# Kernel tuning notes

Measured on AMD Instinct MI355X. Metric: run time of the kernel, lower is better.

Reference implementation:

```python
import jax, jax.numpy as jnp
import numpy as np

MC = 16384
N_STEPS = 120
PERIOD = 30
N_MAT = 4
N_STR = 21
WIDTH_DIFF = 50
WIDTH_VAN = 30
WIDTH_EXO = 20
N_HIDDEN = 3  # n_layers=4 -> input layer + 3 hidden layers + output layer
R = 0.05
TIMEGRID = jnp.asarray(np.linspace(0.0, 1.0, N_STEPS + 1).astype(np.float32))
STRIKES = jnp.asarray(np.linspace(0.8, 1.2, N_STR).astype(np.float32))


def _init_net(key, d_in, width, d_out):
    ks = jax.random.split(key, 6)
    f = lambda k, shape, fan: jax.random.normal(k, shape, jnp.float32) / np.sqrt(fan).astype(np.float32)
    return dict(
        W0=f(ks[0], (N_MAT, d_in, width), d_in),
        b0=f(ks[1], (N_MAT, width), width),
        hW=f(ks[2], (N_MAT, N_HIDDEN, width, width), width),
        hb=f(ks[3], (N_MAT, N_HIDDEN, width), width),
        Wo=f(ks[4], (N_MAT, width, d_out), width),
        bo=f(ks[5], (N_MAT, d_out), width),
    )


def setup_inputs() -> dict:
    key = jax.random.key(0)
    kz, kd, kv, ke = jax.random.split(key, 4)
    inp = {
        "S0": jnp.ones((1,), jnp.float32),
        "z": jax.random.normal(kz, (MC, N_STEPS), jnp.float32),
    }
    for name, net in (("d", _init_net(kd, 2, WIDTH_DIFF, 1)),
                      ("v", _init_net(kv, 2, WIDTH_VAN, N_STR * N_MAT)),
                      ("e", _init_net(ke, N_STEPS + 2, WIDTH_EXO, 1))):
        for pn, arr in net.items():
            inp[name + pn] = arr
    inp["MC_samples"] = MC
    inp["ind_T"] = N_STEPS
    inp["period_length"] = PERIOD
    return inp


def _mlp(x, W0, b0, hW, hb, Wo, bo, softplus_out):
    h = jax.nn.relu(x @ W0 + b0)
    for k in range(hW.shape[0]):  # static small number of hidden layers
        h = jax.nn.relu(h @ hW[k] + hb[k])
    y = h @ Wo + bo
    return jax.nn.softplus(y) if softplus_out else y


def _forward(S0, z, dW0, db0, dhW, dhb, dWo, dbo,
             vW0, vb0, vhW, vhb, vWo, vbo,
             eW0, eb0, ehW, ehb, eWo, ebo,
             MC_samples, ind_T, period_length, remat=False):
    sg = jax.lax.stop_gradient
    S_init = jnp.ones((MC_samples, 1), jnp.float32) * S0
    path0 = jnp.zeros((MC_samples, N_STEPS + 1), jnp.float32).at[:, 0].set(S_init[:, 0])
    zeros_mat = jnp.zeros((N_MAT, N_STR), jnp.float32)

    def step(carry, i):
        S_old, cv_v, cv_e, run_max, path, pv, pvv = carry
        idx = (i - 1) // period_length
        t0 = TIMEGRID[i - 1]
        h = TIMEGRID[i] - TIMEGRID[i - 1]
        sqh = jnp.sqrt(h)
        dWn = sqh * jax.lax.dynamic_slice_in_dim(z, i - 1, 1, 1)  # (MC,1)
        t = jnp.full_like(S_old, t0)
        diff = _mlp(jnp.concatenate([t, S_old], 1),
                    dW0[idx], db0[idx], dhW[idx], dhb[idx], dWo[idx], dbo[idx], True)
        Sd, diffd = sg(S_old), sg(diff)
        S_new = (S_old
                 + R * S_old * h / (1.0 + R * Sd * sqh)
                 + S_old * diff * dWn / (1.0 + Sd * diffd * sqh))
        disc = jnp.exp(-R * t0)
        cv_v = cv_v + disc * Sd * diffd * dWn * _mlp(
            jnp.concatenate([t, Sd], 1),
            vW0[idx], vb0[idx], vhW[idx], vhb[idx], vWo[idx], vbo[idx], False)
        cv_e = cv_e + disc * Sd * diffd * dWn * _mlp(
            jnp.concatenate([t, path], 1),
            eW0[idx], eb0[idx], ehW[idx], ehb[idx], eWo[idx], ebo[idx], False)
        path = jax.lax.dynamic_update_slice(path, sg(S_new), (0, i))
        run_max = jnp.maximum(run_max, S_new)
        # vanilla prices at maturities (i multiple of period_length)
        ind_m = i // period_length - 1
        disc_i = jnp.exp(-R * TIMEGRID[i])
        cv_row = jax.lax.dynamic_slice_in_dim(
            cv_v.reshape(MC_samples, N_MAT, N_STR), ind_m, 1, 1)[:, 0, :]
        pr = disc_i * jnp.maximum(S_new - STRIKES[None, :], 0.0) - cv_row  # (MC, N_STR)
        is_mat = (i % period_length) == 0
        pv = jnp.where(is_mat, jax.lax.dynamic_update_index_in_dim(pv, pr.mean(0), ind_m, 0), pv)
        pvv = jnp.where(is_mat, jax.lax.dynamic_update_index_in_dim(pvv, jnp.var(pr, axis=0, ddof=1), ind_m, 0), pvv)
        return (S_new, cv_v, cv_e, run_max, path, pv, pvv), None

    body = jax.checkpoint(step) if remat else step
    carry0 = (S_init,
              jnp.zeros((MC_samples, N_STR * N_MAT), jnp.float32),
              jnp.zeros((MC_samples, 1), jnp.float32),
              S_init, path0, zeros_mat, zeros_mat)
    (S_T, cv_v, cv_e, run_max, path, pv, pvv), _ = jax.lax.scan(
        body, carry0, jnp.arange(1, ind_T + 1))

    sgv = jax.lax.stop_gradient
    exotic = run_max - S_T
    discT = jnp.exp(-R * TIMEGRID[ind_T])
    e = discT * exotic
    error = sgv(e) - jnp.mean(sgv(e)) - sgv(cv_e)
    price_exo = e - cv_e
    return pv, pvv, price_exo, price_exo.mean(), jnp.var(price_exo, ddof=1), error


def reference(S0, z, dW0, db0, dhW, dhb, dWo, dbo,
              vW0, vb0, vhW, vhb, vWo, vbo,
              eW0, eb0, ehW, ehb, eWo, ebo,
              MC_samples, ind_T, period_length):
    return _forward(S0, z, dW0, db0, dhW, dhb, dWo, dbo,
                    vW0, vb0, vhW, vhb, vWo, vbo,
                    eW0, eb0, ehW, ehb, eWo, ebo,
                    MC_samples, ind_T, period_length)
```

## Files before the change

kernel.cpp:

```cpp
#include <hip/hip_runtime.h>
#include <hip/hip_bf16.h>
#include <math.h>

#define MC      16384
#define NSTEPS  120
#define PER     30
#define NMAT    4
#define NSTR    21
#define RRATE   0.05f
#define NBLK    1024
#define NSAMP   16
#define HSTEP   (1.0f/120.0f)
#define SQH     0.09128709291752769f

typedef short short8  __attribute__((ext_vector_type(8)));
typedef short short4v __attribute__((ext_vector_type(4)));
typedef float f32x4   __attribute__((ext_vector_type(4)));

#define WS_PRPART 0
#define WS_EPART  (NMAT*NSTR*2*NBLK)
#define WS_MEANE  (WS_EPART + NBLK)
#define WS_FRAGS  (WS_MEANE + 3)

#define OUT_PV    0
#define OUT_PVV   84
#define OUT_PEXO  168
#define OUT_MEAN  16552
#define OUT_VAR   16553
#define OUT_ERR   16554

__device__ __forceinline__ float tgridf(int i)  { return (float)i * HSTEP; }
__device__ __forceinline__ float strikef(int s) { return (float)(0.8 + (double)s * 0.02); }
__device__ __forceinline__ float softplusf(float x){
  return fmaxf(x, 0.0f) + __logf(1.0f + __expf(-fabsf(x)));
}
__device__ __forceinline__ unsigned short f2bf(float f){
  __hip_bfloat16 b = __float2bfloat16(f);
  return __builtin_bit_cast(unsigned short, b);
}
__device__ __forceinline__ float bf2f(unsigned short u){
  return __builtin_bit_cast(float, ((unsigned)u)<<16);
}
__device__ __forceinline__ int swaddr(int row, int slot, int inner){
  return row*256 + (((slot + row) & 15) << 4) + inner;
}
__device__ __forceinline__ short8 rdA(const unsigned short* H, int base, int lane){
  int addr = swaddr(lane&15, base + (lane>>4), 0);
  return *(const short8*)((const char*)H + addr);
}
__device__ __forceinline__ f32x4 mm(short8 a, short8 b, f32x4 c){
  return __builtin_amdgcn_mfma_f32_16x16x32_bf16(a, b, c, 0, 0, 0);
}
__device__ __forceinline__ void stD(unsigned short* H, int colbase, int lane,
                                    f32x4 acc, bool relu){
  int col  = colbase + (lane & 15);
  int slot = col >> 3, inner = (col & 7)*2;
  #pragma unroll
  for (int i2=0;i2<4;++i2){
    int rw = ((lane>>4)<<2) + i2;
    float v = acc[i2];
    if (relu) v = fmaxf(v, 0.0f);
    *(unsigned short*)((char*)H + swaddr(rw, slot, inner)) = f2bf(v);
  }
}
__device__ __forceinline__ short8 mkBd(const float* __restrict__ W, const float* __restrict__ bias,
                                       int n0, int kt, int lane){
  short8 r;
  int n = n0 + (lane&15);
  #pragma unroll
  for (int i2=0;i2<8;++i2){
    int k = kt*32 + ((lane>>4)<<3) + i2;
    float w;
    if (k<50)       w = (n<50)? W[k*50+n] : 0.f;
    else if (k==50) w = (n<50)? bias[n] : ((n==50)? 1.f : 0.f);
    else            w = 0.f;
    r[i2] = (short)f2bf(w);
  }
  return r;
}
__device__ __forceinline__ short8 mkBq(const float* __restrict__ W, const float* __restrict__ bias,
                                       int KV, int n0, int lane){
  short8 r;
  int n = n0 + (lane&15);
  #pragma unroll
  for (int i2=0;i2<8;++i2){
    int k = ((lane>>4)<<3) + i2;
    float w;
    if (k<KV)       w = (n<KV)? W[k*KV+n] : 0.f;
    else if (k==KV) w = (n<KV)? bias[n] : ((n==KV)? 1.f : 0.f);
    else            w = 0.f;
    r[i2] = (short)f2bf(w);
  }
  return r;
}

extern "C" __global__ void mk_frags(
    const float* __restrict__ dhW, const float* __restrict__ dhb,
    const float* __restrict__ vhW, const float* __restrict__ vhb,
    const float* __restrict__ ehW, const float* __restrict__ ehb,
    float* __restrict__ ws)
{
  const int bid = blockIdx.x;
  const int p   = bid / 36;
  const int fid = bid % 36;
  const int lane = threadIdx.x;
  short8 fr;
  if (fid < 24){
    int l = fid >> 3, nt = (fid >> 1) & 3, kt = fid & 1;
    fr = mkBd(dhW + p*7500 + l*2500, dhb + p*150 + l*50, nt*16, kt, lane);
  } else if (fid < 30){
    int q = fid - 24, l = q >> 1, nt = q & 1;
    fr = mkBq(vhW + p*2700 + l*900, vhb + p*90 + l*30, 30, nt*16, lane);
  } else {
    int q = fid - 30, l = q >> 1, nt = q & 1;
    fr = mkBq(ehW + p*1200 + l*400, ehb + p*60 + l*20, 20, nt*16, lane);
  }
  ((short8*)(ws + WS_FRAGS))[(p*36 + fid)*64 + lane] = fr;
}

extern "C" __global__ void __launch_bounds__(128,2) mc_main(
    const float* __restrict__ S0p, const float* __restrict__ z,
    const float* __restrict__ dW0, const float* __restrict__ db0,
    const float* __restrict__ dhW, const float* __restrict__ dhb,
    const float* __restrict__ dWo, const float* __restrict__ dbo,
    const float* __restrict__ vW0, const float* __restrict__ vb0,
    const float* __restrict__ vhW, const float* __restrict__ vhb,
    const float* __restrict__ vWo, const float* __restrict__ vbo,
    const float* __restrict__ eW0, const float* __restrict__ eb0,
    const float* __restrict__ ehW, const float* __restrict__ ehb,
    const float* __restrict__ eWo, const float* __restrict__ ebo,
    float* __restrict__ out, float* __restrict__ ws)
{
  __shared__ unsigned short Hb0[NSAMP*128];
  __shared__ unsigned short Hb1[NSAMP*128];
  __shared__ float vh3f[NSAMP*40];
  __shared__ float zper[NSAMP*30];
  __shared__ float eW0per[NMAT*600];
  __shared__ float dW0s[128];
  __shared__ float db0s[64];
  __shared__ float vW0s[64];
  __shared__ float vb0s[32];
  __shared__ float eW0ts[20];
  __shared__ float eb0s[20];
  __shared__ float dWoL[64];
  __shared__ float eWoL[32];
  __shared__ float dtab[PER];
  __shared__ float Sb[NSAMP], ebuf[NSAMP];
  __shared__ float part[84*2];

  const int tid  = threadIdx.x;
  const int lane = tid & 63;
  const int wid  = __builtin_amdgcn_readfirstlane(tid >> 6);
  const int blk  = blockIdx.x;
  const int r    = tid >> 3;
  const int cc   = tid & 7;

  const bool isv = (wid == 0);
  const int  ntA = wid*2, ntB = wid*2+1;

  const float S0v = S0p[0];
  float S = S0v, runmax = S0v, cvE = 0.f;
  f32x4 rr[3];
  #pragma unroll
  for (int q=0;q<3;++q){ rr[q][0]=0.f; rr[q][1]=0.f; rr[q][2]=0.f; rr[q][3]=0.f; }
  float aE[NMAT][4];
  #pragma unroll
  for (int mt2=0;mt2<NMAT;++mt2){ aE[mt2][0]=0.f; aE[mt2][1]=0.f; aE[mt2][2]=0.f; aE[mt2][3]=0.f; }
  float G_[4] = {0.f,0.f,0.f,0.f};

  #pragma unroll 1
  for (int p=0;p<NMAT;++p){
    for (int q=tid; q<NSAMP*30; q+=128){ int r2=q/30, c2=q%30; zper[q] = z[(size_t)(blk*NSAMP+r2)*NSTEPS + p*30 + c2]; }
    for (int q=tid; q<NMAT*600; q+=128){ int mat=q/600, k=q%600; eW0per[q] = eW0[mat*2440 + p*600 + 20 + k]; }
    { int rw = tid>>6, j = tid&63; dW0s[tid] = (j<50)? dW0[p*100 + rw*50 + j] : 0.f; }
    if (tid < 64) db0s[tid] = (tid<50)? db0[p*50+tid] : ((tid==50)? 1.f : 0.f);
    else { int idx = tid-64, rw = idx>>5, j = idx&31; vW0s[idx] = (j<30)? vW0[p*60 + rw*30 + j] : 0.f; }
    if (tid < 32)       vb0s[tid] = (tid<30)? vb0[p*30+tid] : ((tid==30)? 1.f : 0.f);
    else if (tid < 64){ int j=tid-32; if (j<20){ eW0ts[j]=eW0[p*2440+j]; eb0s[j]=eb0[p*20+j]; } }
    else { int j=tid-64; dWoL[j] = (j<50)? dWo[p*50+j] : 0.f; }
    if (tid < 32)       eWoL[tid] = (tid<20)? eWo[p*20+tid] : 0.f;
    else if (tid < 62){ int j=tid-32; dtab[j] = __expf(-RRATE * ((float)(p*PER+j) * HSTEP)); }

    const float dboS = dbo[p], eboS = ebo[p];
    const int fq0 = isv ? 24 : 30;

    __syncthreads();

    #pragma unroll 1
    for (int ii=1; ii<=PER; ++ii){
      const float t0  = tgridf(p*PER + ii - 1);

      const short8* FBp;
      { uintptr_t u = (uintptr_t)(ws + WS_FRAGS); asm volatile("" : "+s"(u));
        FBp = (const short8*)u + (size_t)p*36*64 + lane; }

      {
        short8 hv;
        #pragma unroll
        for (int k=0;k<8;++k){
          int j = cc*8 + k;
          float u = fmaxf(fmaf(t0, dW0s[j], fmaf(S, dW0s[64+j], db0s[j])), 0.f);
          hv[k] = (short)f2bf(u);
        }
        *(short8*)((char*)Hb0 + swaddr(r, cc, 0)) = hv;
        short4v vv;
        #pragma unroll
        for (int k=0;k<4;++k){
          int j = cc*4 + k;
          float u = fmaxf(fmaf(t0, vW0s[j], fmaf(S, vW0s[32+j], vb0s[j])), 0.f);
          vv[k] = (short)f2bf(u);
        }
        *(short4v*)((char*)Hb0 + swaddr(r, 8+(cc>>1), (cc&1)*8)) = vv;
        short4v ev = {0,0,0,0};
        if (cc < 5){
          const int o = (ii-1)*20 + cc*4;
          f32x4 w0 = *(const f32x4*)&eW0per[        o];
          f32x4 w1 = *(const f32x4*)&eW0per[ 600 +  o];
          f32x4 w2 = *(const f32x4*)&eW0per[1200 +  o];
          f32x4 w3 = *(const f32x4*)&eW0per[1800 +  o];
          #pragma unroll
          for (int k=0;k<4;++k){
            aE[0][k] = fmaf(S, w0[k], aE[0][k]);
            aE[1][k] = fmaf(S, w1[k], aE[1][k]);
            aE[2][k] = fmaf(S, w2[k], aE[2][k]);
            aE[3][k] = fmaf(S, w3[k], aE[3][k]);
            float a = (p==0)?aE[0][k]:(p==1)?aE[1][k]:(p==2)?aE[2][k]:aE[3][k];
            int j = cc*4 + k;
            float e0 = fmaxf(t0*eW0ts[j] + a + eb0s[j], 0.f);
            ev[k] = (short)f2bf(e0);
          }
        } else if (cc == 5){
          ev[0] = (short)0x3F80;
        }
        *(short4v*)((char*)Hb0 + swaddr(r, 12+(cc>>1), (cc&1)*8)) = ev;
      }
      __syncthreads();
      {
        short8 bA0 = FBp[(ntA*2+0)*64], bA1 = FBp[(ntA*2+1)*64];
        short8 bB0 = FBp[(ntB*2+0)*64], bB1 = FBp[(ntB*2+1)*64];
        short8 Bq0 = FBp[(fq0+0)*64],   Bq1 = FBp[(fq0+1)*64];
        short8 a0 = rdA(Hb0,0,lane), a1 = rdA(Hb0,4,lane);
        short8 aq = rdA(Hb0, isv?8:12, lane);
        f32x4 c0={0.f,0.f,0.f,0.f}, c1={0.f,0.f,0.f,0.f};
        c0=mm(a0,bA0,c0); c0=mm(a1,bA1,c0);
        c1=mm(a0,bB0,c1); c1=mm(a1,bB1,c1);
        stD(Hb1, ntA*16, lane, c0, true);
        stD(Hb1, ntB*16, lane, c1, true);
        f32x4 cq0={0.f,0.f,0.f,0.f}, cq1={0.f,0.f,0.f,0.f};
        cq0=mm(aq,Bq0,cq0); cq1=mm(aq,Bq1,cq1);
        stD(Hb1, (isv?64:96)+0,  lane, cq0, true);
        stD(Hb1, (isv?64:96)+16, lane, cq1, true);
      }
      __syncthreads();
      {
        short8 bA0 = FBp[(8+ntA*2+0)*64], bA1 = FBp[(8+ntA*2+1)*64];
        short8 bB0 = FBp[(8+ntB*2+0)*64], bB1 = FBp[(8+ntB*2+1)*64];
        short8 Bq0 = FBp[(fq0+2+0)*64],   Bq1 = FBp[(fq0+2+1)*64];
        short8 a0 = rdA(Hb1,0,lane), a1 = rdA(Hb1,4,lane);
        short8 aq = rdA(Hb1, isv?8:12, lane);
        f32x4 c0={0.f,0.f,0.f,0.f}, c1={0.f,0.f,0.f,0.f};
        c0=mm(a0,bA0,c0); c0=mm(a1,bA1,c0);
        c1=mm(a0,bB0,c1); c1=mm(a1,bB1,c1);
        stD(Hb0, ntA*16, lane, c0, true);
        stD(Hb0, ntB*16, lane, c1, true);
        f32x4 cq0={0.f,0.f,0.f,0.f}, cq1={0.f,0.f,0.f,0.f};
        cq0=mm(aq,Bq0,cq0); cq1=mm(aq,Bq1,cq1);
        stD(Hb0, (isv?64:96)+0,  lane, cq0, true);
        stD(Hb0, (isv?64:96)+16, lane, cq1, true);
      }
      __syncthreads();
      {
        short8 bA0 = FBp[(16+ntA*2+0)*64], bA1 = FBp[(16+ntA*2+1)*64];
        short8 bB0 = FBp[(16+ntB*2+0)*64], bB1 = FBp[(16+ntB*2+1)*64];
        short8 Bq0 = FBp[(fq0+4+0)*64],    Bq1 = FBp[(fq0+4+1)*64];
        short8 a0 = rdA(Hb0,0,lane), a1 = rdA(Hb0,4,lane);
        short8 aq = rdA(Hb0, isv?8:12, lane);
        f32x4 c0={0.f,0.f,0.f,0.f}, c1={0.f,0.f,0.f,0.f};
        c0=mm(a0,bA0,c0); c0=mm(a1,bA1,c0);
        c1=mm(a0,bB0,c1); c1=mm(a1,bB1,c1);
        stD(Hb1, ntA*16, lane, c0, true);
        stD(Hb1, ntB*16, lane, c1, true);
        f32x4 cq0={0.f,0.f,0.f,0.f}, cq1={0.f,0.f,0.f,0.f};
        cq0=mm(aq,Bq0,cq0); cq1=mm(aq,Bq1,cq1);
        if (isv){
          #pragma unroll
          for (int i2=0;i2<4;++i2){
            int r0 = ((lane>>4)<<2) + i2;
            vh3f[r0*40 +      (lane&15)] = fmaxf(cq0[i2], 0.f);
            vh3f[r0*40 + 16 + (lane&15)] = fmaxf(cq1[i2], 0.f);
          }
        } else {
          stD(Hb1, 96+0,  lane, cq0, true);
          stD(Hb1, 96+16, lane, cq1, true);
        }
      }
      __syncthreads();
      {
        float yp = 0.f;
        {
          short8 hv = *(const short8*)((const char*)Hb1 + swaddr(r, cc, 0));
          #pragma unroll
          for (int k=0;k<8;++k) yp = fmaf(bf2f((unsigned short)hv[k]), dWoL[cc*8+k], yp);
        }
        float yep = 0.f;
        if (cc < 5){
          short4v hv = *(const short4v*)((const char*)Hb1 + swaddr(r, 12+(cc>>1), (cc&1)*8));
          #pragma unroll
          for (int k=0;k<4;++k) yep = fmaf(bf2f((unsigned short)hv[k]), eWoL[cc*4+k], yep);
        }
        #pragma unroll
        for (int mk=1; mk<8; mk<<=1){ yp += __shfl_xor(yp, mk); yep += __shfl_xor(yep, mk); }
        const float y    = yp + dboS;
        const float diff = softplusf(y);
        const float zv   = zper[r*30 + (ii-1)];
        const float dWn  = SQH * zv;
        const float d1 = 1.f + (RRATE*SQH)*S;
        const float d2 = 1.f + S*diff*SQH;
        const float Snew = S + (RRATE*HSTEP)*S*__builtin_amdgcn_rcpf(d1)
                             + S*diff*dWn*__builtin_amdgcn_rcpf(d2);
        const float disc = dtab[ii-1];
        const float coef = disc * S * diff * dWn;
        cvE = fmaf(coef, yep + eboS, cvE);
        runmax = fmaxf(runmax, Snew);
        {
          f32x4 vv = *(const f32x4*)&vh3f[r*40 + cc*4];
          #pragma unroll
          for (int k=0;k<4;++k) G_[k] = fmaf(coef, vv[k], G_[k]);
        }
        S = Snew;

        if (ii==PER){
          short4v gv;
          #pragma unroll
          for (int k=0;k<4;++k){ gv[k] = (short)f2bf(G_[k]); G_[k] = 0.f; }
          *(short4v*)((char*)Hb0 + swaddr(r, cc>>1, (cc&1)*8)) = gv;
          if (cc==0) Sb[r] = S;
        }
      }

      if (ii==PER){
        __syncthreads();
        const float disc_i = __expf(-RRATE * ((float)(p+1) * 0.25f));
        const float* vWop = vWo + p*2520;
        const float* vbop = vbo + p*84;
        #pragma unroll
        for (int q3=0;q3<3;++q3){
          const int ntr = wid*3 + q3;
          short8 a = rdA(Hb0, 0, lane);
          const int col = ntr*16 + (lane&15);
          short8 bw;
          #pragma unroll
          for (int i2=0;i2<8;++i2){
            int k = ((lane>>4)<<3)+i2;
            float w = 0.f;
            if (col < 84){
              if (k < 30)       w = vWop[k*84+col];
              else if (k == 30) w = vbop[col];
            }
            bw[i2] = (short)f2bf(w);
          }
          f32x4 d4 = {0.f,0.f,0.f,0.f};
          d4 = mm(a,bw,d4);
          const int s = col - p*NSTR;
          const bool inr = (s>=0) && (s<NSTR) && (col<84);
          const float K = strikef(s);
          float ssum=0.f, ssq=0.f;
          #pragma unroll
          for (int i2=0;i2<4;++i2){
            int row = ((lane>>4)<<2) + i2;
            rr[q3][i2] += d4[i2];
            if (inr){
              float pr = disc_i*fmaxf(Sb[row]-K,0.f) - rr[q3][i2];
              ssum += pr; ssq = fmaf(pr,pr,ssq);
            }
          }
          ssum += __shfl_down(ssum,16); ssum += __shfl_down(ssum,32);
          ssq  += __shfl_down(ssq ,16); ssq  += __shfl_down(ssq ,32);
          if (inr && lane<16){
            part[col*2+0] = ssum;
            part[col*2+1] = ssq;
          }
        }
        __syncthreads();
        if (tid < NSTR){
          int cidx = p*NSTR + tid;
          ws[WS_PRPART + (cidx*2+0)*NBLK + blk] = part[cidx*2];
        } else if (tid >= 64 && tid < 64+NSTR){
          int cidx = p*NSTR + (tid-64);
          ws[WS_PRPART + (cidx*2+1)*NBLK + blk] = part[cidx*2+1];
        }
        __syncthreads();
      }
    }
  }

  if (cc==0){
    const float discT = __expf(-RRATE);
    const float e = discT * (runmax - S);
    out[OUT_PEXO + blk*NSAMP + r] = e - cvE;
    ebuf[r] = e;
  }
  __syncthreads();
  if (tid < 16){
    float se = ebuf[tid];
    se += __shfl_down(se,8); se += __shfl_down(se,4);
    se += __shfl_down(se,2); se += __shfl_down(se,1);
    if (tid==0) ws[WS_EPART + blk] = se;
  }
}

extern "C" __global__ void fin_pv(const float* __restrict__ ws, float* __restrict__ out){
  const int t = threadIdx.x;
  if (t >= NMAT*NSTR) return;
  float sum=0.0f, ssq=0.0f;
  for (int b=0;b<NBLK;++b){
    sum += ws[WS_PRPART + (t*2+0)*NBLK + b];
    ssq += ws[WS_PRPART + (t*2+1)*NBLK + b];
  }
  out[OUT_PV  + t] = sum * (1.0f/MC);
  out[OUT_PVV + t] = (ssq - sum*sum*(1.0f/MC)) * (1.0f/(MC-1));
}

extern "C" __global__ void fin_pe(float* out, float* ws){
  __shared__ float sA[4], sB[4], sC[4];
  const int t = threadIdx.x;
  float sum=0.0f, ssq=0.0f;
  for (int idx=t; idx<MC; idx+=256){
    const float v = out[OUT_PEXO+idx];
    sum += v; ssq = fmaf(v,v,ssq);
  }
  float es = 0.0f;
  for (int idx=t; idx<NBLK; idx+=256) es += ws[WS_EPART + idx];
  for (int o=32;o>0;o>>=1){
    sum += __shfl_down(sum,o);
    ssq += __shfl_down(ssq,o);
    es  += __shfl_down(es,o);
  }
  const int w=t>>6, lane=t&63;
  if (lane==0){ sA[w]=sum; sB[w]=ssq; sC[w]=es; }
  __syncthreads();
  if (t==0){
    const float s=sA[0]+sA[1]+sA[2]+sA[3];
    const float q=sB[0]+sB[1]+sB[2]+sB[3];
    const float e=sC[0]+sC[1]+sC[2]+sC[3];
    out[OUT_MEAN]=s*(1.0f/MC);
    out[OUT_VAR]=(q - s*s*(1.0f/MC))*(1.0f/(MC-1));
    ws[WS_MEANE]=e*(1.0f/MC);
  }
}

extern "C" __global__ void fin_err(float* out, const float* __restrict__ ws){
  const int m = blockIdx.x*blockDim.x + threadIdx.x;
  if (m < MC) out[OUT_ERR+m] = out[OUT_PEXO+m] - ws[WS_MEANE];
}

extern "C" void kernel_launch(void* const* d_in, const int* in_sizes, int n_in,
                              void* d_out, int out_size, void* d_ws, size_t ws_size,
                              hipStream_t stream){
  (void)in_sizes; (void)n_in; (void)out_size; (void)ws_size;
  const float* S0 =(const float*)d_in[0];
  const float* z  =(const float*)d_in[1];
  const float* dW0=(const float*)d_in[2];
  const float* db0=(const float*)d_in[3];
  const float* dhW=(const float*)d_in[4];
  const float* dhb=(const float*)d_in[5];
  const float* dWo=(const float*)d_in[6];
  const float* dbo=(const float*)d_in[7];
  const float* vW0=(const float*)d_in[8];
  const float* vb0=(const float*)d_in[9];
  const float* vhW=(const float*)d_in[10];
  const float* vhb=(const float*)d_in[11];
  const float* vWo=(const float*)d_in[12];
  const float* vbo=(const float*)d_in[13];
  const float* eW0=(const float*)d_in[14];
  const float* eb0=(const float*)d_in[15];
  const float* ehW=(const float*)d_in[16];
  const float* ehb=(const float*)d_in[17];
  const float* eWo=(const float*)d_in[18];
  const float* ebo=(const float*)d_in[19];
  float* out=(float*)d_out;
  float* ws =(float*)d_ws;

  mk_frags<<<dim3(NMAT*36),dim3(64),0,stream>>>(dhW,dhb,vhW,vhb,ehW,ehb,ws);
  mc_main<<<dim3(NBLK),dim3(128),0,stream>>>(S0,z,dW0,db0,dhW,dhb,dWo,dbo,
                                             vW0,vb0,vhW,vhb,vWo,vbo,
                                             eW0,eb0,ehW,ehb,eWo,ebo,out,ws);
  fin_pv <<<dim3(1), dim3(128),0,stream>>>(ws,out);
  fin_pe <<<dim3(1), dim3(256),0,stream>>>(out,ws);
  fin_err<<<dim3(64),dim3(256),0,stream>>>(out,ws);
}
```

Baseline: 447.6 us.

## Halve samples per block, double grid, store exotic weights in bf16, parallelise fin_pv

Each block now handles 8 samples instead of 16, doubling the grid to 2048 blocks. Threads are remapped to 16 per sample row so the per-thread layer-0 and output work is halved. MFMA tiles stay 16 rows wide and half the rows are zero padding, so matrix-core work per sample doubles. The eW0 slice in shared memory is stored as bf16 to cut LDS use, and launch bounds are raised to 4 blocks per CU for higher occupancy. The fin_pv reduction is spread over 84 blocks with a wave-level shuffle reduce instead of a serial loop over blocks.

After: 763.4 us. 70.6% more time.

```diff
diff --git a/kernel.cpp b/kernel.cpp
--- a/kernel.cpp
+++ b/kernel.cpp
@@ -8,8 +8,8 @@
 #define NMAT    4
 #define NSTR    21
 #define RRATE   0.05f
-#define NBLK    1024
-#define NSAMP   16
+#define NBLK    2048
+#define NSAMP   8
 #define HSTEP   (1.0f/120.0f)
 #define SQH     0.09128709291752769f
 
@@ -20,7 +20,7 @@
 #define WS_PRPART 0
 #define WS_EPART  (NMAT*NSTR*2*NBLK)
 #define WS_MEANE  (WS_EPART + NBLK)
-#define WS_FRAGS  (WS_MEANE + 3)
+#define WS_FRAGS  346116
 
 #define OUT_PV    0
 #define OUT_PVV   84
@@ -40,6 +40,9 @@
 }
 __device__ __forceinline__ float bf2f(unsigned short u){
   return __builtin_bit_cast(float, ((unsigned)u)<<16);
+}
+__device__ __forceinline__ unsigned pk2(float a, float b){
+  return (unsigned)f2bf(a) | ((unsigned)f2bf(b)<<16);
 }
 __device__ __forceinline__ int swaddr(int row, int slot, int inner){
   return row*256 + (((slot + row) & 15) << 4) + inner;
@@ -118,7 +121,7 @@
   ((short8*)(ws + WS_FRAGS))[(p*36 + fid)*64 + lane] = fr;
 }
 
-extern "C" __global__ void __launch_bounds__(128,2) mc_main(
+extern "C" __global__ void __launch_bounds__(128,4) mc_main(
     const float* __restrict__ S0p, const float* __restrict__ z,
     const float* __restrict__ dW0, const float* __restrict__ db0,
     const float* __restrict__ dhW, const float* __restrict__ dhb,
@@ -131,11 +134,11 @@
     const float* __restrict__ eWo, const float* __restrict__ ebo,
     float* __restrict__ out, float* __restrict__ ws)
 {
-  __shared__ unsigned short Hb0[NSAMP*128];
-  __shared__ unsigned short Hb1[NSAMP*128];
-  __shared__ float vh3f[NSAMP*40];
+  __shared__ unsigned short Hb0[16*128];
+  __shared__ unsigned short Hb1[16*128];
+  __shared__ float vh3f[16*40];
   __shared__ float zper[NSAMP*30];
-  __shared__ float eW0per[NMAT*600];
+  __shared__ unsigned short eW0perb[NMAT*600];
   __shared__ float dW0s[128];
   __shared__ float db0s[64];
   __shared__ float vW0s[64];
@@ -152,8 +155,10 @@
   const int lane = tid & 63;
   const int wid  = __builtin_amdgcn_readfirstlane(tid >> 6);
   const int blk  = blockIdx.x;
-  const int r    = tid >> 3;
-  const int cc   = tid & 7;
+  const int r    = tid >> 4;
+  const int cc   = tid & 15;
+
+  for (int q=tid; q<16*128; q+=128){ Hb0[q]=0; Hb1[q]=0; }
 
   const bool isv = (wid == 0);
   const int  ntA = wid*2, ntB = wid*2+1;
@@ -163,21 +168,21 @@
   f32x4 rr[3];
   #pragma unroll
   for (int q=0;q<3;++q){ rr[q][0]=0.f; rr[q][1]=0.f; rr[q][2]=0.f; rr[q][3]=0.f; }
-  float aE[NMAT][4];
+  float aE[NMAT][2];
   #pragma unroll
-  for (int mt2=0;mt2<NMAT;++mt2){ aE[mt2][0]=0.f; aE[mt2][1]=0.f; aE[mt2][2]=0.f; aE[mt2][3]=0.f; }
-  float G_[4] = {0.f,0.f,0.f,0.f};
+  for (int mt2=0;mt2<NMAT;++mt2){ aE[mt2][0]=0.f; aE[mt2][1]=0.f; }
+  float G0=0.f, G1=0.f;
 
   #pragma unroll 1
   for (int p=0;p<NMAT;++p){
     for (int q=tid; q<NSAMP*30; q+=128){ int r2=q/30, c2=q%30; zper[q] = z[(size_t)(blk*NSAMP+r2)*NSTEPS + p*30 + c2]; }
-    for (int q=tid; q<NMAT*600; q+=128){ int mat=q/600, k=q%600; eW0per[q] = eW0[mat*2440 + p*600 + 20 + k]; }
+    for (int q=tid; q<NMAT*600; q+=128){ int mat=q/600, k=q%600; eW0perb[q] = f2bf(eW0[mat*2440 + p*600 + 20 + k]); }
     { int rw = tid>>6, j = tid&63; dW0s[tid] = (j<50)? dW0[p*100 + rw*50 + j] : 0.f; }
     if (tid < 64) db0s[tid] = (tid<50)? db0[p*50+tid] : ((tid==50)? 1.f : 0.f);
     else { int idx = tid-64, rw = idx>>5, j = idx&31; vW0s[idx] = (j<30)? vW0[p*60 + rw*30 + j] : 0.f; }
     if (tid < 32)       vb0s[tid] = (tid<30)? vb0[p*30+tid] : ((tid==30)? 1.f : 0.f);
-    else if (tid < 64){ int j=tid-32; if (j<20){ eW0ts[j]=eW0[p*2440+j]; eb0s[j]=eb0[p*20+j]; } }
-    else { int j=tid-64; dWoL[j] = (j<50)? dWo[p*50+j] : 0.f; }
+    else if (tid < 52){ int j=tid-32; eW0ts[j]=eW0[p*2440+j]; eb0s[j]=eb0[p*20+j]; }
+    else if (tid >= 64){ int j=tid-64; dWoL[j] = (j<50)? dWo[p*50+j] : 0.f; }
     if (tid < 32)       eWoL[tid] = (tid<20)? eWo[p*20+tid] : 0.f;
     else if (tid < 62){ int j=tid-32; dtab[j] = __expf(-RRATE * ((float)(p*PER+j) * HSTEP)); }
 
@@ -195,44 +200,45 @@
         FBp = (const short8*)u + (size_t)p*36*64 + lane; }
 
       {
-        short8 hv;
-        #pragma unroll
-        for (int k=0;k<8;++k){
-          int j = cc*8 + k;
-          float u = fmaxf(fmaf(t0, dW0s[j], fmaf(S, dW0s[64+j], db0s[j])), 0.f);
-          hv[k] = (short)f2bf(u);
-        }
-        *(short8*)((char*)Hb0 + swaddr(r, cc, 0)) = hv;
-        short4v vv;
+        short4v hv;
         #pragma unroll
         for (int k=0;k<4;++k){
           int j = cc*4 + k;
-          float u = fmaxf(fmaf(t0, vW0s[j], fmaf(S, vW0s[32+j], vb0s[j])), 0.f);
-          vv[k] = (short)f2bf(u);
-        }
-        *(short4v*)((char*)Hb0 + swaddr(r, 8+(cc>>1), (cc&1)*8)) = vv;
-        short4v ev = {0,0,0,0};
-        if (cc < 5){
-          const int o = (ii-1)*20 + cc*4;
-          f32x4 w0 = *(const f32x4*)&eW0per[        o];
-          f32x4 w1 = *(const f32x4*)&eW0per[ 600 +  o];
-          f32x4 w2 = *(const f32x4*)&eW0per[1200 +  o];
-          f32x4 w3 = *(const f32x4*)&eW0per[1800 +  o];
-          #pragma unroll
-          for (int k=0;k<4;++k){
-            aE[0][k] = fmaf(S, w0[k], aE[0][k]);
-            aE[1][k] = fmaf(S, w1[k], aE[1][k]);
-            aE[2][k] = fmaf(S, w2[k], aE[2][k]);
-            aE[3][k] = fmaf(S, w3[k], aE[3][k]);
-            float a = (p==0)?aE[0][k]:(p==1)?aE[1][k]:(p==2)?aE[2][k]:aE[3][k];
-            int j = cc*4 + k;
-            float e0 = fmaxf(t0*eW0ts[j] + a + eb0s[j], 0.f);
-            ev[k] = (short)f2bf(e0);
-          }
-        } else if (cc == 5){
-          ev[0] = (short)0x3F80;
-        }
-        *(short4v*)((char*)Hb0 + swaddr(r, 12+(cc>>1), (cc&1)*8)) = ev;
+          float u = fmaxf(fmaf(t0, dW0s[j], fmaf(S, dW0s[64+j], db0s[j])), 0.f);
+          hv[k] = (short)f2bf(u);
+        }
+        *(short4v*)((char*)Hb0 + swaddr(r, cc>>1, (cc&1)*8)) = hv;
+        {
+          int j = cc*2;
+          float u0 = fmaxf(fmaf(t0, vW0s[j],   fmaf(S, vW0s[32+j],   vb0s[j])),   0.f);
+          float u1 = fmaxf(fmaf(t0, vW0s[j+1], fmaf(S, vW0s[32+j+1], vb0s[j+1])), 0.f);
+          *(unsigned*)((char*)Hb0 + swaddr(r, 8+(cc>>2), (cc&3)*4)) = pk2(u0,u1);
+        }
+        unsigned ev = 0;
+        if (cc < 10){
+          const int o = (ii-1)*20 + cc*2;
+          unsigned p0 = *(const unsigned*)&eW0perb[        o];
+          unsigned p1 = *(const unsigned*)&eW0perb[ 600 +  o];
+          unsigned p2 = *(const unsigned*)&eW0perb[1200 +  o];
+          unsigned p3 = *(const unsigned*)&eW0perb[1800 +  o];
+          aE[0][0] = fmaf(S, bf2f((unsigned short)(p0&0xffff)), aE[0][0]);
+          aE[0][1] = fmaf(S, bf2f((unsigned short)(p0>>16)),    aE[0][1]);
+          aE[1][0] = fmaf(S, bf2f((unsigned short)(p1&0xffff)), aE[1][0]);
+          aE[1][1] = fmaf(S, bf2f((unsigned short)(p1>>16)),    aE[1][1]);
+          aE[2][0] = fmaf(S, bf2f((unsigned short)(p2&0xffff)), aE[2][0]);
+          aE[2][1] = fmaf(S, bf2f((unsigned short)(p2>>16)),    aE[2][1]);
+          aE[3][0] = fmaf(S, bf2f((unsigned short)(p3&0xffff)), aE[3][0]);
+          aE[3][1] = fmaf(S, bf2f((unsigned short)(p3>>16)),    aE[3][1]);
+          float a0 = (p==0)?aE[0][0]:(p==1)?aE[1][0]:(p==2)?aE[2][0]:aE[3][0];
+          float a1 = (p==0)?aE[0][1]:(p==1)?aE[1][1]:(p==2)?aE[2][1]:aE[3][1];
+          int j = cc*2;
+          float e0 = fmaxf(t0*eW0ts[j]   + a0 + eb0s[j],   0.f);
+          float e1 = fmaxf(t0*eW0ts[j+1] + a1 + eb0s[j+1], 0.f);
+          ev = pk2(e0,e1);
+        } else if (cc == 10){
+          ev = 0x3F80u;
+        }
+        *(unsigned*)((char*)Hb0 + swaddr(r, 12+(cc>>2), (cc&3)*4)) = ev;
       }
       __syncthreads();
       {
@@ -298,18 +304,18 @@
       {
         float yp = 0.f;
         {
-          short8 hv = *(const short8*)((const char*)Hb1 + swaddr(r, cc, 0));
+          short4v hv = *(const short4v*)((const char*)Hb1 + swaddr(r, cc>>1, (cc&1)*8));
           #pragma unroll
-          for (int k=0;k<8;++k) yp = fmaf(bf2f((unsigned short)hv[k]), dWoL[cc*8+k], yp);
+          for (int k=0;k<4;++k) yp = fmaf(bf2f((unsigned short)hv[k]), dWoL[cc*4+k], yp);
         }
         float yep = 0.f;
-        if (cc < 5){
-          short4v hv = *(const short4v*)((const char*)Hb1 + swaddr(r, 12+(cc>>1), (cc&1)*8));
-          #pragma unroll
-          for (int k=0;k<4;++k) yep = fmaf(bf2f((unsigned short)hv[k]), eWoL[cc*4+k], yep);
+        if (cc < 10){
+          unsigned hv = *(const unsigned*)((const char*)Hb1 + swaddr(r, 12+(cc>>2), (cc&3)*4));
+          yep = fmaf(bf2f((unsigned short)(hv&0xffff)), eWoL[cc*2],   yep);
+          yep = fmaf(bf2f((unsigned short)(hv>>16)),    eWoL[cc*2+1], yep);
         }
         #pragma unroll
-        for (int mk=1; mk<8; mk<<=1){ yp += __shfl_xor(yp, mk); yep += __shfl_xor(yep, mk); }
+        for (int mk=1; mk<16; mk<<=1){ yp += __shfl_xor(yp, mk); yep += __shfl_xor(yep, mk); }
         const float y    = yp + dboS;
         const float diff = softplusf(y);
         const float zv   = zper[r*30 + (ii-1)];
@@ -323,17 +329,15 @@
         cvE = fmaf(coef, yep + eboS, cvE);
         runmax = fmaxf(runmax, Snew);
         {
-          f32x4 vv = *(const f32x4*)&vh3f[r*40 + cc*4];
-          #pragma unroll
-          for (int k=0;k<4;++k) G_[k] = fmaf(coef, vv[k], G_[k]);
+          float2 vv = *(const float2*)&vh3f[r*40 + cc*2];
+          G0 = fmaf(coef, vv.x, G0);
+          G1 = fmaf(coef, vv.y, G1);
         }
         S = Snew;
 
         if (ii==PER){
-          short4v gv;
-          #pragma unroll
-          for (int k=0;k<4;++k){ gv[k] = (short)f2bf(G_[k]); G_[k] = 0.f; }
-          *(short4v*)((char*)Hb0 + swaddr(r, cc>>1, (cc&1)*8)) = gv;
+          *(unsigned*)((char*)Hb0 + swaddr(r, cc>>2, (cc&3)*4)) = pk2(G0,G1);
+          G0=0.f; G1=0.f;
           if (cc==0) Sb[r] = S;
         }
       }
@@ -369,7 +373,7 @@
           for (int i2=0;i2<4;++i2){
             int row = ((lane>>4)<<2) + i2;
             rr[q3][i2] += d4[i2];
-            if (inr){
+            if (row < NSAMP && inr){
               float pr = disc_i*fmaxf(Sb[row]-K,0.f) - rr[q3][i2];
               ssum += pr; ssq = fmaf(pr,pr,ssq);
             }
@@ -401,24 +405,26 @@
     ebuf[r] = e;
   }
   __syncthreads();
-  if (tid < 16){
+  if (tid < NSAMP){
     float se = ebuf[tid];
-    se += __shfl_down(se,8); se += __shfl_down(se,4);
-    se += __shfl_down(se,2); se += __shfl_down(se,1);
+    se += __shfl_down(se,4); se += __shfl_down(se,2); se += __shfl_down(se,1);
     if (tid==0) ws[WS_EPART + blk] = se;
   }
 }
 
 extern "C" __global__ void fin_pv(const float* __restrict__ ws, float* __restrict__ out){
-  const int t = threadIdx.x;
-  if (t >= NMAT*NSTR) return;
+  const int t    = blockIdx.x;
+  const int lane = threadIdx.x;
   float sum=0.0f, ssq=0.0f;
-  for (int b=0;b<NBLK;++b){
+  for (int b=lane; b<NBLK; b+=64){
     sum += ws[WS_PRPART + (t*2+0)*NBLK + b];
     ssq += ws[WS_PRPART + (t*2+1)*NBLK + b];
   }
-  out[OUT_PV  + t] = sum * (1.0f/MC);
-  out[OUT_PVV + t] = (ssq - sum*sum*(1.0f/MC)) * (1.0f/(MC-1));
+  for (int o=32;o>0;o>>=1){ sum += __shfl_down(sum,o); ssq += __shfl_down(ssq,o); }
+  if (lane==0){
+    out[OUT_PV  + t] = sum * (1.0f/MC);
+    out[OUT_PVV + t] = (ssq - sum*sum*(1.0f/MC)) * (1.0f/(MC-1));
+  }
 }
 
 extern "C" __global__ void fin_pe(float* out, float* ws){
@@ -485,7 +491,7 @@
   mc_main<<<dim3(NBLK),dim3(128),0,stream>>>(S0,z,dW0,db0,dhW,dhb,dWo,dbo,
                                              vW0,vb0,vhW,vhb,vWo,vbo,
                                              eW0,eb0,ehW,ehb,eWo,ebo,out,ws);
-  fin_pv <<<dim3(1), dim3(128),0,stream>>>(ws,out);
+  fin_pv <<<dim3(84), dim3(64),0,stream>>>(ws,out);
   fin_pe <<<dim3(1), dim3(256),0,stream>>>(out,ws);
   fin_err<<<dim3(64),dim3(256),0,stream>>>(out,ws);
 }
```

## Fuse output-layer dot products into last MFMA layer and prefetch weight fragments

Applied to the files above, without the earlier changes.

The last hidden layer's MFMA results are now multiplied directly by the output weights in registers and reduced with cross-lane shuffles into small shared arrays. This skips storing bf16 activations to LDS and re-reading them for the output projection. Weight fragments for the next layer are also loaded from global memory before each barrier so the loads overlap the sync. The output sum now uses fp32 activations instead of bf16-rounded ones, which slightly changes numerics, and the prefetched fragments raise register pressure. WS_FRAGS is hardcoded to a constant offset.

Result: faster. 418.1 us, median of 2 (-6.6%).

```diff
diff --git a/kernel.cpp b/kernel.cpp
--- a/kernel.cpp
+++ b/kernel.cpp
@@ -20,7 +20,7 @@
 #define WS_PRPART 0
 #define WS_EPART  (NMAT*NSTR*2*NBLK)
 #define WS_MEANE  (WS_EPART + NBLK)
-#define WS_FRAGS  (WS_MEANE + 3)
+#define WS_FRAGS  173060
 
 #define OUT_PV    0
 #define OUT_PVV   84
@@ -146,6 +146,8 @@
   __shared__ float eWoL[32];
   __shared__ float dtab[PER];
   __shared__ float Sb[NSAMP], ebuf[NSAMP];
+  __shared__ float ydp[2][NSAMP];
+  __shared__ float ype[NSAMP];
   __shared__ float part[84*2];
 
   const int tid  = threadIdx.x;
@@ -186,6 +188,11 @@
 
     __syncthreads();
 
+    const float wdA = dWoL[ntA*16 + (lane&15)];
+    const float wdB = dWoL[ntB*16 + (lane&15)];
+    const float weA = eWoL[lane&15];
+    const float weB = eWoL[16 + (lane&15)];
+
     #pragma unroll 1
     for (int ii=1; ii<=PER; ++ii){
       const float t0  = tgridf(p*PER + ii - 1);
@@ -193,6 +200,10 @@
       const short8* FBp;
       { uintptr_t u = (uintptr_t)(ws + WS_FRAGS); asm volatile("" : "+s"(u));
         FBp = (const short8*)u + (size_t)p*36*64 + lane; }
+
+      short8 xA0 = FBp[(ntA*2+0)*64], xA1 = FBp[(ntA*2+1)*64];
+      short8 xB0 = FBp[(ntB*2+0)*64], xB1 = FBp[(ntB*2+1)*64];
+      short8 xQ0 = FBp[(fq0+0)*64],   xQ1 = FBp[(fq0+1)*64];
 
       {
         short8 hv;
@@ -235,53 +246,62 @@
         *(short4v*)((char*)Hb0 + swaddr(r, 12+(cc>>1), (cc&1)*8)) = ev;
       }
       __syncthreads();
+      short8 yA0 = FBp[(8+ntA*2+0)*64], yA1 = FBp[(8+ntA*2+1)*64];
+      short8 yB0 = FBp[(8+ntB*2+0)*64], yB1 = FBp[(8+ntB*2+1)*64];
+      short8 yQ0 = FBp[(fq0+2+0)*64],   yQ1 = FBp[(fq0+2+1)*64];
       {
-        short8 bA0 = FBp[(ntA*2+0)*64], bA1 = FBp[(ntA*2+1)*64];
-        short8 bB0 = FBp[(ntB*2+0)*64], bB1 = FBp[(ntB*2+1)*64];
-        short8 Bq0 = FBp[(fq0+0)*64],   Bq1 = FBp[(fq0+1)*64];
         short8 a0 = rdA(Hb0,0,lane), a1 = rdA(Hb0,4,lane);
         short8 aq = rdA(Hb0, isv?8:12, lane);
         f32x4 c0={0.f,0.f,0.f,0.f}, c1={0.f,0.f,0.f,0.f};
-        c0=mm(a0,bA0,c0); c0=mm(a1,bA1,c0);
-        c1=mm(a0,bB0,c1); c1=mm(a1,bB1,c1);
+        c0=mm(a0,xA0,c0); c0=mm(a1,xA1,c0);
+        c1=mm(a0,xB0,c1); c1=mm(a1,xB1,c1);
         stD(Hb1, ntA*16, lane, c0, true);
         stD(Hb1, ntB*16, lane, c1, true);
         f32x4 cq0={0.f,0.f,0.f,0.f}, cq1={0.f,0.f,0.f,0.f};
-        cq0=mm(aq,Bq0,cq0); cq1=mm(aq,Bq1,cq1);
+        cq0=mm(aq,xQ0,cq0); cq1=mm(aq,xQ1,cq1);
         stD(Hb1, (isv?64:96)+0,  lane, cq0, true);
         stD(Hb1, (isv?64:96)+16, lane, cq1, true);
       }
       __syncthreads();
+      short8 zA0 = FBp[(16+ntA*2+0)*64], zA1 = FBp[(16+ntA*2+1)*64];
+      short8 zB0 = FBp[(16+ntB*2+0)*64], zB1 = FBp[(16+ntB*2+1)*64];
+      short8 zQ0 = FBp[(fq0+4+0)*64],    zQ1 = FBp[(fq0+4+1)*64];
       {
-        short8 bA0 = FBp[(8+ntA*2+0)*64], bA1 = FBp[(8+ntA*2+1)*64];
-        short8 bB0 = FBp[(8+ntB*2+0)*64], bB1 = FBp[(8+ntB*2+1)*64];
-        short8 Bq0 = FBp[(fq0+2+0)*64],   Bq1 = FBp[(fq0+2+1)*64];
         short8 a0 = rdA(Hb1,0,lane), a1 = rdA(Hb1,4,lane);
         short8 aq = rdA(Hb1, isv?8:12, lane);
         f32x4 c0={0.f,0.f,0.f,0.f}, c1={0.f,0.f,0.f,0.f};
-        c0=mm(a0,bA0,c0); c0=mm(a1,bA1,c0);
-        c1=mm(a0,bB0,c1); c1=mm(a1,bB1,c1);
+        c0=mm(a0,yA0,c0); c0=mm(a1,yA1,c0);
+        c1=mm(a0,yB0,c1); c1=mm(a1,yB1,c1);
         stD(Hb0, ntA*16, lane, c0, true);
         stD(Hb0, ntB*16, lane, c1, true);
         f32x4 cq0={0.f,0.f,0.f,0.f}, cq1={0.f,0.f,0.f,0.f};
-        cq0=mm(aq,Bq0,cq0); cq1=mm(aq,Bq1,cq1);
+        cq0=mm(aq,yQ0,cq0); cq1=mm(aq,yQ1,cq1);
         stD(Hb0, (isv?64:96)+0,  lane, cq0, true);
         stD(Hb0, (isv?64:96)+16, lane, cq1, true);
       }
       __syncthreads();
       {
-        short8 bA0 = FBp[(16+ntA*2+0)*64], bA1 = FBp[(16+ntA*2+1)*64];
-        short8 bB0 = FBp[(16+ntB*2+0)*64], bB1 = FBp[(16+ntB*2+1)*64];
-        short8 Bq0 = FBp[(fq0+4+0)*64],    Bq1 = FBp[(fq0+4+1)*64];
         short8 a0 = rdA(Hb0,0,lane), a1 = rdA(Hb0,4,lane);
         short8 aq = rdA(Hb0, isv?8:12, lane);
         f32x4 c0={0.f,0.f,0.f,0.f}, c1={0.f,0.f,0.f,0.f};
-        c0=mm(a0,bA0,c0); c0=mm(a1,bA1,c0);
-        c1=mm(a0,bB0,c1); c1=mm(a1,bB1,c1);
-        stD(Hb1, ntA*16, lane, c0, true);
-        stD(Hb1, ntB*16, lane, c1, true);
+        c0=mm(a0,zA0,c0); c0=mm(a1,zA1,c0);
+        c1=mm(a0,zB0,c1); c1=mm(a1,zB1,c1);
+        f32x4 pd;
+        #pragma unroll
+        for (int i2=0;i2<4;++i2)
+          pd[i2] = fmaf(fmaxf(c0[i2],0.f), wdA, fmaxf(c1[i2],0.f)*wdB);
         f32x4 cq0={0.f,0.f,0.f,0.f}, cq1={0.f,0.f,0.f,0.f};
-        cq0=mm(aq,Bq0,cq0); cq1=mm(aq,Bq1,cq1);
+        cq0=mm(aq,zQ0,cq0); cq1=mm(aq,zQ1,cq1);
+        #pragma unroll
+        for (int mk=1; mk<16; mk<<=1){
+          #pragma unroll
+          for (int i2=0;i2<4;++i2) pd[i2] += __shfl_xor(pd[i2], mk);
+        }
+        if ((lane&15)==0){
+          int rg = (lane>>4)<<2;
+          #pragma unroll
+          for (int i2=0;i2<4;++i2) ydp[wid][rg+i2] = pd[i2];
+        }
         if (isv){
           #pragma unroll
           for (int i2=0;i2<4;++i2){
@@ -290,27 +310,26 @@
             vh3f[r0*40 + 16 + (lane&15)] = fmaxf(cq1[i2], 0.f);
           }
         } else {
-          stD(Hb1, 96+0,  lane, cq0, true);
-          stD(Hb1, 96+16, lane, cq1, true);
+          f32x4 pe;
+          #pragma unroll
+          for (int i2=0;i2<4;++i2)
+            pe[i2] = fmaf(fmaxf(cq0[i2],0.f), weA, fmaxf(cq1[i2],0.f)*weB);
+          #pragma unroll
+          for (int mk=1; mk<16; mk<<=1){
+            #pragma unroll
+            for (int i2=0;i2<4;++i2) pe[i2] += __shfl_xor(pe[i2], mk);
+          }
+          if ((lane&15)==0){
+            int rg = (lane>>4)<<2;
+            #pragma unroll
+            for (int i2=0;i2<4;++i2) ype[rg+i2] = pe[i2];
+          }
         }
       }
       __syncthreads();
       {
-        float yp = 0.f;
-        {
-          short8 hv = *(const short8*)((const char*)Hb1 + swaddr(r, cc, 0));
-          #pragma unroll
-          for (int k=0;k<8;++k) yp = fmaf(bf2f((unsigned short)hv[k]), dWoL[cc*8+k], yp);
-        }
-        float yep = 0.f;
-        if (cc < 5){
-          short4v hv = *(const short4v*)((const char*)Hb1 + swaddr(r, 12+(cc>>1), (cc&1)*8));
-          #pragma unroll
-          for (int k=0;k<4;++k) yep = fmaf(bf2f((unsigned short)hv[k]), eWoL[cc*4+k], yep);
-        }
-        #pragma unroll
-        for (int mk=1; mk<8; mk<<=1){ yp += __shfl_xor(yp, mk); yep += __shfl_xor(yep, mk); }
-        const float y    = yp + dboS;
+        const float y    = ydp[0][r] + ydp[1][r] + dboS;
+        const float yep  = ype[r];
         const float diff = softplusf(y);
         const float zv   = zper[r*30 + (ii-1)];
         const float dWn  = SQH * zv;
```
